# Kernel tuning notes

Measured on AMD Instinct MI355X. Metric: run time of the kernel, lower is better.

## Reference

```python
import jax, jax.numpy as jnp
import numpy as np

NUM_HEADS = 12


def setup_inputs() -> dict:
    key = jax.random.key(0)
    ks = jax.random.split(key, 7)
    B, H, W, C = 1, 64, 64, 768
    hd = C // NUM_HEADS
    return {
        "x": jax.random.normal(ks[0], (B, H, W, C), dtype=jnp.float32),
        "qkv_w": jax.random.normal(ks[1], (C, 3 * C), dtype=jnp.float32) * 0.02,
        "qkv_b": jax.random.normal(ks[2], (3 * C,), dtype=jnp.float32) * 0.02,
        "proj_w": jax.random.normal(ks[3], (C, C), dtype=jnp.float32) * 0.02,
        "proj_b": jax.random.normal(ks[4], (C,), dtype=jnp.float32) * 0.02,
        "rel_pos_h": jax.random.normal(ks[5], (2 * H - 1, hd), dtype=jnp.float32) * 0.02,
        "rel_pos_w": jax.random.normal(ks[6], (2 * W - 1, hd), dtype=jnp.float32) * 0.02,
    }


def _rel_table(size, rel_pos):
    # q_size == k_size so relative_coords = i - j + (size - 1)
    coords = jnp.arange(size)[:, None] - jnp.arange(size)[None, :] + (size - 1)
    return rel_pos[coords]  # [size, size, head_dim]


def reference(x, qkv_w, qkv_b, proj_w, proj_b, rel_pos_h, rel_pos_w):
    B, H, W, C = x.shape
    nh = NUM_HEADS
    hd = C // nh
    scale = hd ** -0.5
    N = H * W

    qkv = x.reshape(B, N, C) @ qkv_w + qkv_b  # [B, N, 3C]
    qkv = qkv.reshape(B, N, 3, nh, hd).transpose(2, 0, 3, 1, 4).reshape(3, B * nh, N, hd)
    q, k, v = qkv[0], qkv[1], qkv[2]

    attn = jnp.einsum("bqd,bkd->bqk", q * scale, k)  # [B*nh, N, N]

    # decomposed relative position bias
    Rh = _rel_table(H, rel_pos_h)  # [H, H, hd]
    Rw = _rel_table(W, rel_pos_w)  # [W, W, hd]
    qr = q.reshape(B * nh, H, W, hd)
    rel_h = jnp.einsum("bhwc,hkc->bhwk", qr, Rh)  # [B*nh, H, W, H]
    rel_w = jnp.einsum("bhwc,wkc->bhwk", qr, Rw)  # [B*nh, H, W, W]
    bias = rel_h[..., :, None] + rel_w[..., None, :]  # [B*nh, H, W, H, W]
    attn = attn + bias.reshape(B * nh, N, N)

    attn = jax.nn.softmax(attn, axis=-1)
    out = jnp.einsum("bqk,bkd->bqd", attn, v)  # [B*nh, N, hd]
    out = out.reshape(B, nh, H, W, hd).transpose(0, 2, 3, 1, 4).reshape(B, H, W, C)
    return out @ proj_w + proj_b
```

## Files before the change

kernel.cpp:

```cpp
#include <hip/hip_runtime.h>
#include <math.h>

#define NHEADS 12
#define NTOK 4096
#define LOG2E 1.44269504f

typedef __attribute__((ext_vector_type(8))) short bf8v;
typedef __attribute__((ext_vector_type(4))) float f4v;
typedef __attribute__((ext_vector_type(16))) float f16v;

__device__ __forceinline__ unsigned short f2bf(float f) {
  unsigned int u = __float_as_uint(f);
  u += 0x7fffu + ((u >> 16) & 1u);
  return (unsigned short)(u >> 16);
}
__device__ __forceinline__ bf8v pack8(float4 a, float4 b) {
  bf8v v;
  v[0] = (short)f2bf(a.x); v[1] = (short)f2bf(a.y);
  v[2] = (short)f2bf(a.z); v[3] = (short)f2bf(a.w);
  v[4] = (short)f2bf(b.x); v[5] = (short)f2bf(b.y);
  v[6] = (short)f2bf(b.z); v[7] = (short)f2bf(b.w);
  return v;
}
__device__ __forceinline__ unsigned pkbf(float hi, float lo) {
  return __builtin_amdgcn_perm(__float_as_uint(hi) + 0x8000u,
                               __float_as_uint(lo) + 0x8000u, 0x07060302u);
}
__device__ __forceinline__ unsigned cvtpk(float lo, float hi) {
  unsigned r;
  asm("v_cvt_pk_bf16_f32 %0, %1, %2" : "=v"(r) : "v"(lo), "v"(hi));
  return r;
}
__device__ __forceinline__ void gload_lds16(const void* g, void* l) {
  __builtin_amdgcn_global_load_lds(
      (const __attribute__((address_space(1))) void*)g,
      (__attribute__((address_space(3))) void*)l, 16, 0, 0);
}

__device__ __forceinline__ void tcvt_body(
    const float* __restrict__ in, short* __restrict__ out, int R, int C,
    int bx, int by, int t, float (*Ts)[65])
{
    const int bc = bx * 64, br = by * 64;
    {
        const int r = t >> 2, c0 = (t & 3) * 16;
        const float* src = in + (size_t)(br + r) * C + bc + c0;
#pragma unroll
        for (int i = 0; i < 4; ++i) {
            float4 a = *(const float4*)(src + 4 * i);
            Ts[r][c0 + 4 * i + 0] = a.x;
            Ts[r][c0 + 4 * i + 1] = a.y;
            Ts[r][c0 + 4 * i + 2] = a.z;
            Ts[r][c0 + 4 * i + 3] = a.w;
        }
    }
    __syncthreads();
    const int c = t >> 2, r0 = (t & 3) * 16;
    short* dst = out + (size_t)(bc + c) * R + br + r0;
#pragma unroll
    for (int p = 0; p < 2; ++p) {
        bf8v v;
#pragma unroll
        for (int i = 0; i < 8; ++i) v[i] = (short)f2bf(Ts[r0 + p * 8 + i][c]);
        *(bf8v*)(dst + p * 8) = v;
    }
}

__global__ __launch_bounds__(256) void prep_kernel(
    const float* __restrict__ x, const float* __restrict__ qkvw,
    const float* __restrict__ pw, short* __restrict__ xh,
    short* __restrict__ wqkvT, short* __restrict__ pwT)
{
    __shared__ float Ts[64][65];
    const int bid = blockIdx.x, t = threadIdx.x;
    if (bid < 1536) {
        const size_t i = ((size_t)bid * 256 + t) * 8;
        float4 a = *(const float4*)(x + i);
        float4 b = *(const float4*)(x + i + 4);
        *(bf8v*)(xh + i) = pack8(a, b);
    } else if (bid < 1968) {
        const int idx = bid - 1536;
        tcvt_body(qkvw, wqkvT, 768, 2304, idx % 36, idx / 36, t, Ts);
    } else {
        const int idx = bid - 1968;
        tcvt_body(pw, pwT, 768, 768, idx % 12, idx / 12, t, Ts);
    }
}

__global__ __launch_bounds__(256) void qkv_mfma_kernel(
    const short* __restrict__ xh, const short* __restrict__ wT,
    const float* __restrict__ bias, short* __restrict__ qbh,
    short* __restrict__ kblk, short* __restrict__ vblk)
{
    __shared__ __align__(16) short As[128 * 32];
    __shared__ __align__(16) short Bs[96 * 32];
    const int t = threadIdx.x;
    const int w = t >> 6, lane = t & 63;
    const int l15 = lane & 15, l4 = lane >> 4;
    const int wr = w >> 1, wc = w & 1;
    const int row0 = blockIdx.y * 128, col0 = blockIdx.x * 96;
    const int ldr = lane >> 2;
    const int ldk = (lane & 3) * 8;

    f4v acc[4][3] = {};
    const short* aBase = xh + (size_t)(row0 + w * 32 + ldr) * 768 + ldk;
    const short* bBase0 = wT + (size_t)(col0 + w * 16 + ldr) * 768 + ldk;
    const short* bBase1 = wT + (size_t)(col0 + 64 + w * 16 + ldr) * 768 + ldk;

    for (int kk = 0; kk < 768; kk += 32) {
        __syncthreads();
#pragma unroll
        for (int c = 0; c < 2; ++c)
            gload_lds16(aBase + (size_t)c * 16 * 768 + kk,
                        &As[(w * 32 + c * 16) * 32]);
        gload_lds16(bBase0 + kk, &Bs[(w * 16) * 32]);
        if (w < 2)
            gload_lds16(bBase1 + kk, &Bs[(64 + w * 16) * 32]);
        __syncthreads();
        bf8v af[4], bg[3];
#pragma unroll
        for (int i = 0; i < 4; ++i)
            af[i] = *(const bf8v*)&As[(wr * 64 + 16 * i + l15) * 32 + l4 * 8];
#pragma unroll
        for (int j = 0; j < 3; ++j)
            bg[j] = *(const bf8v*)&Bs[(wc * 48 + 16 * j + l15) * 32 + l4 * 8];
#pragma unroll
        for (int i = 0; i < 4; ++i)
#pragma unroll
            for (int j = 0; j < 3; ++j)
                acc[i][j] = __builtin_amdgcn_mfma_f32_16x16x32_bf16(
                    af[i], bg[j], acc[i][j], 0, 0, 0);
    }

#pragma unroll
    for (int j = 0; j < 3; ++j) {
        const int n = col0 + wc * 48 + 16 * j + l15;
        const int s = n / 768;
        const int rm = n - s * 768;
        const int h = rm >> 6, d = rm & 63;
        const float bv = bias[n];
        if (s == 2) {
#pragma unroll
            for (int i = 0; i < 4; ++i) {
                const int m = row0 + wr * 64 + 16 * i + l4 * 4;
                short4 pv;
                pv.x = (short)f2bf(acc[i][j][0] + bv);
                pv.y = (short)f2bf(acc[i][j][1] + bv);
                pv.z = (short)f2bf(acc[i][j][2] + bv);
                pv.w = (short)f2bf(acc[i][j][3] + bv);
                *(short4*)(vblk +
                           ((size_t)(h * 256 + (m >> 4)) * 64 + d) * 16 +
                           (m & 15)) = pv;
            }
        } else if (s == 0) {
#pragma unroll
            for (int i = 0; i < 4; ++i) {
                const int m = row0 + wr * 64 + 16 * i + l4 * 4;
#pragma unroll
                for (int r = 0; r < 4; ++r)
                    qbh[((size_t)h * NTOK + m + r) * 64 + d] =
                        (short)f2bf(acc[i][j][r] + bv);
            }
        } else {
#pragma unroll
            for (int i = 0; i < 4; ++i) {
                const int m = row0 + wr * 64 + 16 * i + l4 * 4;
                short* dst = kblk +
                    ((((size_t)(h * 128 + (m >> 5)) * 8 + (d >> 3)) * 32 +
                      (m & 31)) * 8 + (d & 7));
#pragma unroll
                for (int r = 0; r < 4; ++r)
                    dst[r * 8] = (short)f2bf(acc[i][j][r] + bv);
            }
        }
    }
}

union FlashSMem {
    float relHs[64][65];
    float U[128 * 65];
    struct {
        float OEp[64][64];
        float lEp[64];
    };
};

__global__ __launch_bounds__(256, 3) void flash_mfma_kernel(
    const short* __restrict__ qbh, const short* __restrict__ kblk,
    const short* __restrict__ vblk, const float* __restrict__ rpw,
    const float* __restrict__ rph, short* __restrict__ aob)
{
    __shared__ __align__(16) FlashSMem sm;

    const int t = threadIdx.x;
    const int qt = blockIdx.x, head = blockIdx.y;
    const int row0 = qt * 64;
    const int lane = t & 63, w = t >> 6;
    const int qh2 = w & 1, th = w >> 1;
    const int l31 = lane & 31, hf = lane >> 5;
    const size_t hB = (size_t)head * NTOK * 64;
    const float SC = 0.125f * LOG2E;

    const int q = row0 + qh2 * 32 + l31;
    bf8v bQ[4];
    {
        const short* qsrc = qbh + hB + (size_t)q * 64;
#pragma unroll
        for (int ks = 0; ks < 4; ++ks)
            bQ[ks] = *(const bf8v*)(qsrc + ks * 16 + hf * 8);
    }

    const short* kb = kblk + (size_t)head * 262144 + th * 4096 + hf * 256 +
                      (size_t)l31 * 8;
    bf8v kf[2][4];
#pragma unroll
    for (int t32 = 0; t32 < 2; ++t32)
#pragma unroll
        for (int ks = 0; ks < 4; ++ks)
            kf[t32][ks] = *(const bf8v*)(kb + t32 * 2048 + ks * 512);

    const short* vb2 = vblk + ((size_t)head * 256 * 64 + l31) * 16 + hf * 8;

#pragma unroll
    for (int jt2 = 0; jt2 < 2; ++jt2) {
        const int jt = 2 * th + jt2;
        int j = jt * 32 + l31;
        if (j > 126) j = 0;
        const float* asrc = rpw + (size_t)j * 64;
        f16v c = {};
#pragma unroll
        for (int ks = 0; ks < 4; ++ks) {
            float4 u0 = *(const float4*)(asrc + ks * 16 + hf * 8);
            float4 u1 = *(const float4*)(asrc + ks * 16 + hf * 8 + 4);
            c = __builtin_amdgcn_mfma_f32_32x32x16_bf16(
                pack8(u0, u1), bQ[ks], c, 0, 0, 0);
        }
#pragma unroll
        for (int reg = 0; reg < 16; ++reg)
            sm.U[(jt * 32 + (reg & 3) + 8 * (reg >> 2) + 4 * hf) * 65 +
                 qh2 * 32 + l31] = c[reg];
    }
    __syncthreads();
    const int qw = qh2 * 32 + l31;
    uint2 rwp[2][4];
#pragma unroll
    for (int t32 = 0; t32 < 2; ++t32)
#pragma unroll
        for (int g = 0; g < 4; ++g) {
            const int kw = t32 * 32 + 8 * g + 4 * hf;
            const float v0 = sm.U[(qw + 63 - kw) * 65 + qw] * LOG2E;
            const float v1 = sm.U[(qw + 62 - kw) * 65 + qw] * LOG2E;
            const float v2 = sm.U[(qw + 61 - kw) * 65 + qw] * LOG2E;
            const float v3 = sm.U[(qw + 60 - kw) * 65 + qw] * LOG2E;
            rwp[t32][g].x = pkbf(v1, v0);
            rwp[t32][g].y = pkbf(v3, v2);
        }
    __syncthreads();

    {
        const int kh = th * 32 + l31;
        const float* asrc = rph + (size_t)(qt + 63 - kh) * 64;
        f16v c = {};
#pragma unroll
        for (int ks = 0; ks < 4; ++ks) {
            float4 u0 = *(const float4*)(asrc + ks * 16 + hf * 8);
            float4 u1 = *(const float4*)(asrc + ks * 16 + hf * 8 + 4);
            u0.x *= LOG2E; u0.y *= LOG2E; u0.z *= LOG2E; u0.w *= LOG2E;
            u1.x *= LOG2E; u1.y *= LOG2E; u1.z *= LOG2E; u1.w *= LOG2E;
            c = __builtin_amdgcn_mfma_f32_32x32x16_bf16(
                pack8(u0, u1), bQ[ks], c, 0, 0, 0);
        }
#pragma unroll
        for (int reg = 0; reg < 16; ++reg)
            sm.relHs[th * 32 + (reg & 3) + 8 * (reg >> 2) + 4 * hf]
                    [qh2 * 32 + l31] = c[reg];
    }
    __syncthreads();

    f16v O[2] = {{}, {}};
    float lsum = 0.f;

#pragma unroll 1
    for (int it = 0; it < 32; ++it) {
        bf8v vB[2][2][2];
        {
            const short* vit = vb2 + (size_t)(it * 8 + th * 4) * 1024;
#pragma unroll
            for (int t32 = 0; t32 < 2; ++t32)
#pragma unroll
                for (int ks2 = 0; ks2 < 2; ++ks2)
#pragma unroll
                    for (int nt = 0; nt < 2; ++nt)
                        vB[t32][ks2][nt] = *(const bf8v*)(
                            vit + ((size_t)(t32 * 2 + ks2) * 64 + nt * 32) *
                                      16);
        }
        const float rh = sm.relHs[2 * it + th][qw];

        __builtin_amdgcn_s_setprio(1);
        f16v acc[2] = {{}, {}};
#pragma unroll
        for (int ks = 0; ks < 4; ++ks)
#pragma unroll
            for (int t32 = 0; t32 < 2; ++t32)
                acc[t32] = __builtin_amdgcn_mfma_f32_32x32x16_bf16(
                    kf[t32][ks], bQ[ks], acc[t32], 0, 0, 0);
        __builtin_amdgcn_s_setprio(0);

        {
            const short* kp = kb + (size_t)(it + 1) * 8192;
#pragma unroll
            for (int t32 = 0; t32 < 2; ++t32)
#pragma unroll
                for (int ks = 0; ks < 4; ++ks)
                    kf[t32][ks] =
                        *(const bf8v*)(kp + t32 * 2048 + ks * 512);
        }

        unsigned xg[2][4], yg[2][4];
#pragma unroll
        for (int t32 = 0; t32 < 2; ++t32) {
            float sub = 0.f;
#pragma unroll
            for (int g = 0; g < 4; ++g) {
                const unsigned u0 = rwp[t32][g].x;
                const unsigned u1 = rwp[t32][g].y;
                const float b0 = __uint_as_float(u0 << 16) + rh;
                const float b1 = __uint_as_float(u0 & 0xffff0000u) + rh;
                const float b2 = __uint_as_float(u1 << 16) + rh;
                const float b3 = __uint_as_float(u1 & 0xffff0000u) + rh;
                const float e0 = __builtin_amdgcn_exp2f(
                    fmaf(acc[t32][4 * g + 0], SC, b0));
                const float e1 = __builtin_amdgcn_exp2f(
                    fmaf(acc[t32][4 * g + 1], SC, b1));
                const float e2 = __builtin_amdgcn_exp2f(
                    fmaf(acc[t32][4 * g + 2], SC, b2));
                const float e3 = __builtin_amdgcn_exp2f(
                    fmaf(acc[t32][4 * g + 3], SC, b3));
                sub += (e0 + e1) + (e2 + e3);
                xg[t32][g] = cvtpk(e0, e1);
                yg[t32][g] = cvtpk(e2, e3);
            }
            lsum += sub;
        }

        __builtin_amdgcn_s_setprio(1);
#pragma unroll
        for (int t32 = 0; t32 < 2; ++t32)
#pragma unroll
            for (int ks2 = 0; ks2 < 2; ++ks2) {
                auto px = __builtin_amdgcn_permlane32_swap(
                    xg[t32][2 * ks2], xg[t32][2 * ks2 + 1], false, false);
                auto py = __builtin_amdgcn_permlane32_swap(
                    yg[t32][2 * ks2], yg[t32][2 * ks2 + 1], false, false);
                int4 av;
                av.x = (int)px[0];
                av.y = (int)py[0];
                av.z = (int)px[1];
                av.w = (int)py[1];
                union { int4 i; bf8v v; } u; u.i = av;
#pragma unroll
                for (int nt = 0; nt < 2; ++nt)
                    O[nt] = __builtin_amdgcn_mfma_f32_32x32x16_bf16(
                        u.v, vB[t32][ks2][nt], O[nt], 0, 0, 0);
            }
        __builtin_amdgcn_s_setprio(0);
    }

    lsum += __shfl_xor(lsum, 32);
    __syncthreads();
    if (th == 1) {
#pragma unroll
        for (int nt = 0; nt < 2; ++nt)
#pragma unroll
            for (int reg = 0; reg < 16; ++reg) {
                const int qr = (reg & 3) + 8 * (reg >> 2) + 4 * hf;
                sm.OEp[qh2 * 32 + qr][nt * 32 + l31] = O[nt][reg];
            }
        if (lane < 32) sm.lEp[qh2 * 32 + l31] = lsum;
    }
    __syncthreads();
    if (th == 0) {
        lsum += sm.lEp[qh2 * 32 + l31];
        const float linv = 1.0f / lsum;
#pragma unroll
        for (int nt = 0; nt < 2; ++nt)
#pragma unroll
            for (int reg = 0; reg < 16; ++reg) {
                const int qr = (reg & 3) + 8 * (reg >> 2) + 4 * hf;
                const float li = __shfl(linv, qr);
                const float o =
                    O[nt][reg] + sm.OEp[qh2 * 32 + qr][nt * 32 + l31];
                aob[(size_t)(row0 + qh2 * 32 + qr) * 768 + head * 64 +
                    nt * 32 + l31] = (short)f2bf(o * li);
            }
    }
}

__global__ __launch_bounds__(256) void proj_mfma_kernel(
    const short* __restrict__ aoh, const short* __restrict__ pwT,
    const float* __restrict__ bias, float* __restrict__ out)
{
    __shared__ __align__(16) short As[64 * 32];
    __shared__ __align__(16) short Bs[64 * 32];
    const int t = threadIdx.x;
    const int w = t >> 6, lane = t & 63;
    const int l15 = lane & 15, l4 = lane >> 4;
    const int wr = w >> 1, wc = w & 1;
    const int row0 = blockIdx.y * 64, col0 = blockIdx.x * 64;
    const int ldr = lane >> 2;
    const int ldk = (lane & 3) * 8;

    f4v acc[2][2] = {};
    const short* aBase = aoh + (size_t)(row0 + w * 16 + ldr) * 768 + ldk;
    const short* bBase = pwT + (size_t)(col0 + w * 16 + ldr) * 768 + ldk;

    for (int kk = 0; kk < 768; kk += 32) {
        __syncthreads();
        gload_lds16(aBase + kk, &As[(w * 16) * 32]);
        gload_lds16(bBase + kk, &Bs[(w * 16) * 32]);
        __syncthreads();
        bf8v af[2], bg[2];
#pragma unroll
        for (int i = 0; i < 2; ++i)
            af[i] = *(const bf8v*)&As[(wr * 32 + 16 * i + l15) * 32 + l4 * 8];
#pragma unroll
        for (int j = 0; j < 2; ++j)
            bg[j] = *(const bf8v*)&Bs[(wc * 32 + 16 * j + l15) * 32 + l4 * 8];
#pragma unroll
        for (int i = 0; i < 2; ++i)
#pragma unroll
            for (int j = 0; j < 2; ++j)
                acc[i][j] = __builtin_amdgcn_mfma_f32_16x16x32_bf16(
                    af[i], bg[j], acc[i][j], 0, 0, 0);
    }

#pragma unroll
    for (int j = 0; j < 2; ++j) {
        const int n = col0 + wc * 32 + 16 * j + l15;
        const float bv = bias[n];
#pragma unroll
        for (int i = 0; i < 2; ++i) {
            const int m = row0 + wr * 32 + 16 * i + l4 * 4;
#pragma unroll
            for (int r = 0; r < 4; ++r)
                out[(size_t)(m + r) * 768 + n] = acc[i][j][r] + bv;
        }
    }
}

extern "C" void kernel_launch(void* const* d_in, const int* in_sizes, int n_in,
                              void* d_out, int out_size, void* d_ws,
                              size_t ws_size, hipStream_t stream)
{
    (void)in_sizes; (void)n_in; (void)out_size; (void)ws_size;
    const float* x    = (const float*)d_in[0];
    const float* qkvw = (const float*)d_in[1];
    const float* qkvb = (const float*)d_in[2];
    const float* pw   = (const float*)d_in[3];
    const float* pb   = (const float*)d_in[4];
    const float* rph  = (const float*)d_in[5];
    const float* rpw  = (const float*)d_in[6];
    float* out = (float*)d_out;

    const size_t S = (size_t)NHEADS * NTOK * 64;
    short* qbh  = (short*)d_ws;
    short* kblk = qbh + S;
    short* vblk = kblk + S;
    short* xh   = vblk + S;
    short* aob  = xh;
    short* wqkvT = xh + S;
    short* pwT  = wqkvT + (size_t)2304 * 768;

    prep_kernel<<<dim3(2112), 256, 0, stream>>>(x, qkvw, pw, xh, wqkvT, pwT);
    qkv_mfma_kernel<<<dim3(24, 32), 256, 0, stream>>>(xh, wqkvT, qkvb,
                                                      qbh, kblk, vblk);
    flash_mfma_kernel<<<dim3(64, NHEADS), 256, 0, stream>>>(qbh, kblk, vblk,
                                                            rpw, rph, aob);
    proj_mfma_kernel<<<dim3(12, 64), 256, 0, stream>>>(aob, pwT, pb, out);
}
```

Measured before the change: 260.6 us.

## Split flash attention keys across two blocks and combine partial outputs

Flash attention now runs on a third grid dimension of 2, with each block handling half the key tiles. Unnormalised partial outputs and row sums go to fp32 workspace, and a new combine kernel adds them, normalises and writes bf16. This doubles the number of blocks (768 to 1536) to fill the GPU better, at the cost of extra global traffic, an extra launch, and repeated per-block setup such as the relative-position tables. The loop is also reordered and the setprio hints are removed. The split is safe without max tracking because the softmax does not subtract a running maximum.

```diff
diff --git a/kernel.cpp b/kernel.cpp
--- a/kernel.cpp
+++ b/kernel.cpp
@@ -188,12 +188,13 @@
 __global__ __launch_bounds__(256, 3) void flash_mfma_kernel(
     const short* __restrict__ qbh, const short* __restrict__ kblk,
     const short* __restrict__ vblk, const float* __restrict__ rpw,
-    const float* __restrict__ rph, short* __restrict__ aob)
+    const float* __restrict__ rph, float* __restrict__ opart,
+    float* __restrict__ lsums)
 {
     __shared__ __align__(16) FlashSMem sm;
 
     const int t = threadIdx.x;
-    const int qt = blockIdx.x, head = blockIdx.y;
+    const int qt = blockIdx.x, head = blockIdx.y, zz = blockIdx.z;
     const int row0 = qt * 64;
     const int lane = t & 63, w = t >> 6;
     const int qh2 = w & 1, th = w >> 1;
@@ -217,7 +218,8 @@
     for (int t32 = 0; t32 < 2; ++t32)
 #pragma unroll
         for (int ks = 0; ks < 4; ++ks)
-            kf[t32][ks] = *(const bf8v*)(kb + t32 * 2048 + ks * 512);
+            kf[t32][ks] = *(const bf8v*)(kb + (size_t)zz * 131072 +
+                                         t32 * 2048 + ks * 512);
 
     const short* vb2 = vblk + ((size_t)head * 256 * 64 + l31) * 16 + hf * 8;
 
@@ -280,8 +282,15 @@
     f16v O[2] = {{}, {}};
     float lsum = 0.f;
 
-#pragma unroll 1
-    for (int it = 0; it < 32; ++it) {
+    for (int it = zz * 16; it < zz * 16 + 16; ++it) {
+        f16v acc[2] = {{}, {}};
+#pragma unroll
+        for (int ks = 0; ks < 4; ++ks)
+#pragma unroll
+            for (int t32 = 0; t32 < 2; ++t32)
+                acc[t32] = __builtin_amdgcn_mfma_f32_32x32x16_bf16(
+                    kf[t32][ks], bQ[ks], acc[t32], 0, 0, 0);
+
         bf8v vB[2][2][2];
         {
             const short* vit = vb2 + (size_t)(it * 8 + th * 4) * 1024;
@@ -295,17 +304,6 @@
                             vit + ((size_t)(t32 * 2 + ks2) * 64 + nt * 32) *
                                       16);
         }
-        const float rh = sm.relHs[2 * it + th][qw];
-
-        __builtin_amdgcn_s_setprio(1);
-        f16v acc[2] = {{}, {}};
-#pragma unroll
-        for (int ks = 0; ks < 4; ++ks)
-#pragma unroll
-            for (int t32 = 0; t32 < 2; ++t32)
-                acc[t32] = __builtin_amdgcn_mfma_f32_32x32x16_bf16(
-                    kf[t32][ks], bQ[ks], acc[t32], 0, 0, 0);
-        __builtin_amdgcn_s_setprio(0);
 
         {
             const short* kp = kb + (size_t)(it + 1) * 8192;
@@ -316,6 +314,8 @@
                     kf[t32][ks] =
                         *(const bf8v*)(kp + t32 * 2048 + ks * 512);
         }
+
+        const float rh = sm.relHs[2 * it + th][qw];
 
         unsigned xg[2][4], yg[2][4];
 #pragma unroll
@@ -344,7 +344,6 @@
             lsum += sub;
         }
 
-        __builtin_amdgcn_s_setprio(1);
 #pragma unroll
         for (int t32 = 0; t32 < 2; ++t32)
 #pragma unroll
@@ -364,7 +363,6 @@
                     O[nt] = __builtin_amdgcn_mfma_f32_32x32x16_bf16(
                         u.v, vB[t32][ks2][nt], O[nt], 0, 0, 0);
             }
-        __builtin_amdgcn_s_setprio(0);
     }
 
     lsum += __shfl_xor(lsum, 32);
@@ -382,18 +380,45 @@
     __syncthreads();
     if (th == 0) {
         lsum += sm.lEp[qh2 * 32 + l31];
-        const float linv = 1.0f / lsum;
 #pragma unroll
         for (int nt = 0; nt < 2; ++nt)
 #pragma unroll
             for (int reg = 0; reg < 16; ++reg) {
                 const int qr = (reg & 3) + 8 * (reg >> 2) + 4 * hf;
-                const float li = __shfl(linv, qr);
-                const float o =
+                opart[((size_t)(zz * NTOK) + row0 + qh2 * 32 + qr) * 768 +
+                      head * 64 + nt * 32 + l31] =
                     O[nt][reg] + sm.OEp[qh2 * 32 + qr][nt * 32 + l31];
-                aob[(size_t)(row0 + qh2 * 32 + qr) * 768 + head * 64 +
-                    nt * 32 + l31] = (short)f2bf(o * li);
-            }
+            }
+        if (lane < 32)
+            lsums[(size_t)zz * (NHEADS * NTOK) + head * NTOK + row0 +
+                  qh2 * 32 + l31] = lsum;
+    }
+}
+
+__global__ __launch_bounds__(256) void ocomb_kernel(
+    const float* __restrict__ opart, const float* __restrict__ lsums,
+    short* __restrict__ aob)
+{
+    const int t = threadIdx.x;
+    const int wv = t >> 6, lane = t & 63;
+    const int tok = blockIdx.x * 4 + wv;
+    const float* o0 = opart + (size_t)tok * 768;
+    const float* o1 = opart + (size_t)(NTOK + tok) * 768;
+#pragma unroll
+    for (int c = 0; c < 3; ++c) {
+        const int col = (lane + c * 64) * 4;
+        const int h = col >> 6;
+        const float l = lsums[(size_t)h * NTOK + tok] +
+                        lsums[(size_t)(NHEADS + h) * NTOK + tok];
+        const float li = 1.0f / l;
+        float4 a = *(const float4*)(o0 + col);
+        float4 b = *(const float4*)(o1 + col);
+        short4 r;
+        r.x = (short)f2bf((a.x + b.x) * li);
+        r.y = (short)f2bf((a.y + b.y) * li);
+        r.z = (short)f2bf((a.z + b.z) * li);
+        r.w = (short)f2bf((a.w + b.w) * li);
+        *(short4*)(aob + (size_t)tok * 768 + col) = r;
     }
 }
 
@@ -471,11 +496,14 @@
     short* aob  = xh;
     short* wqkvT = xh + S;
     short* pwT  = wqkvT + (size_t)2304 * 768;
+    float* opart = (float*)(pwT + (size_t)768 * 768);
+    float* lsums = opart + (size_t)2 * NTOK * 768;
 
     prep_kernel<<<dim3(2112), 256, 0, stream>>>(x, qkvw, pw, xh, wqkvT, pwT);
     qkv_mfma_kernel<<<dim3(24, 32), 256, 0, stream>>>(xh, wqkvT, qkvb,
                                                       qbh, kblk, vblk);
-    flash_mfma_kernel<<<dim3(64, NHEADS), 256, 0, stream>>>(qbh, kblk, vblk,
-                                                            rpw, rph, aob);
+    flash_mfma_kernel<<<dim3(64, NHEADS, 2), 256, 0, stream>>>(
+        qbh, kblk, vblk, rpw, rph, opart, lsums);
+    ocomb_kernel<<<dim3(NTOK / 4), 256, 0, stream>>>(opart, lsums, aob);
     proj_mfma_kernel<<<dim3(12, 64), 256, 0, stream>>>(aob, pwT, pb, out);
 }
```

Measured after the change: 233.6 us. -10.4%, faster.
